# Kernel optimization log

Hardware: AMD Instinct MI355X
Metric: run time of the kernel (lower is better)

## Reference

```python
import jax, jax.numpy as jnp
import numpy as np

B, C, H, W = 4, 128, 128, 128
K = 9          # 3x3 kernel taps
TAU, BETA = 0.5, 10.0


def conv3x3(x, w, b):
    # x: (B,Cin,H,W), w: (Cout,Cin,3,3), stride 1, padding 1
    y = jax.lax.conv_general_dilated(
        x, w, window_strides=(1, 1), padding=((1, 1), (1, 1)),
        dimension_numbers=('NCHW', 'OIHW', 'NCHW'))
    return y + b[None, :, None, None]


def bilinear_sample(x, py, px):
    # x: (B,C,H,W); py,px: (B,K,H,W) fractional coords -> (B,C,K,H,W), zero outside
    Hi, Wi = x.shape[2], x.shape[3]
    y0 = jnp.floor(py); x0 = jnp.floor(px)
    y1 = y0 + 1.0;      x1 = x0 + 1.0
    ly = py - y0; lx = px - x0
    hy = 1.0 - ly; hx = 1.0 - lx
    xf = x.reshape(x.shape[0], x.shape[1], -1)  # (B,C,HW)

    def corner(yc, xc, wgt):
        valid = (yc >= 0) & (yc <= Hi - 1) & (xc >= 0) & (xc <= Wi - 1)
        yi = jnp.clip(yc, 0, Hi - 1).astype(jnp.int32)
        xi = jnp.clip(xc, 0, Wi - 1).astype(jnp.int32)
        idx = (yi * Wi + xi).reshape(yc.shape[0], -1)  # (B, K*H*W)
        g = jax.vmap(lambda f, i: f[:, i])(xf, idx)    # (B,C,K*H*W)
        g = g.reshape(x.shape[0], x.shape[1], *yc.shape[1:])  # (B,C,K,H,W)
        return g * (wgt * valid.astype(wgt.dtype))[:, None]

    return (corner(y0, x0, hy * hx) + corner(y0, x1, hy * lx)
            + corner(y1, x0, ly * hx) + corner(y1, x1, ly * lx))


def modulated_dcn(x, offset, mask, w, b):
    # offset: (B,2K,H,W) layout (dy,dx) per tap; mask: (B,K,H,W)
    Bn, Cn, Hn, Wn = x.shape
    off = offset.reshape(Bn, K, 2, Hn, Wn)
    dy, dx = off[:, :, 0], off[:, :, 1]
    ky, kx = jnp.meshgrid(jnp.arange(3), jnp.arange(3), indexing='ij')
    base_y = (ky.reshape(-1) - 1).astype(x.dtype)  # dilation=1, padding=1, stride=1
    base_x = (kx.reshape(-1) - 1).astype(x.dtype)
    hh = jnp.arange(Hn, dtype=x.dtype)
    ww = jnp.arange(Wn, dtype=x.dtype)
    py = hh[None, None, :, None] + base_y[None, :, None, None] + dy  # (B,K,H,W)
    px = ww[None, None, None, :] + base_x[None, :, None, None] + dx
    samp = bilinear_sample(x, py, px) * mask[:, None]  # (B,C,K,H,W)
    out = jnp.einsum('bckhw,ock->bohw', samp, w.reshape(w.shape[0], w.shape[1], K))
    return out + b[None, :, None, None]


def setup_inputs() -> dict:
    key = jax.random.key(0)
    ks = jax.random.split(key, 8)
    x = jax.random.normal(ks[0], (B, C, H, W), dtype=jnp.float32)
    U = jax.random.uniform(ks[1], (B, 1, H, W), dtype=jnp.float32)
    # conv_offset_mask: (3*K, C+1, 3, 3); small scale -> offsets of O(1) pixel
    w_om = jax.random.normal(ks[2], (3 * K, C + 1, 3, 3), dtype=jnp.float32) * 0.01
    b_om = jnp.zeros((3 * K,), dtype=jnp.float32)
    kaiming = float(np.sqrt(2.0 / (C * 9)))
    w_dcn = jax.random.normal(ks[3], (C, C, 3, 3), dtype=jnp.float32) * kaiming
    b_dcn = jnp.zeros((C,), dtype=jnp.float32)
    w1 = jax.random.normal(ks[4], (C, C, 3, 3), dtype=jnp.float32) * kaiming
    b1 = jnp.zeros((C,), dtype=jnp.float32)
    w2 = jax.random.normal(ks[5], (C, C, 3, 3), dtype=jnp.float32) * float(np.sqrt(1.0 / (C * 9)))
    b2 = jnp.zeros((C,), dtype=jnp.float32)
    return {"x": x, "U": U, "w_om": w_om, "b_om": b_om, "w_dcn": w_dcn,
            "b_dcn": b_dcn, "w1": w1, "b1": b1, "w2": w2, "b2": b2}


def reference(x, U, w_om, b_om, w_dcn, b_dcn, w1, b1, w2, b2):
    U = jnp.clip(U, 0.0, 1.0)
    guide = jnp.concatenate([x, U], axis=1)                # (B,C+1,H,W)
    om = conv3x3(guide, w_om, b_om)                        # (B,3K,H,W)
    offset = om[:, :2 * K]
    mask = 2.0 * jax.nn.sigmoid(om[:, 2 * K:])
    z = modulated_dcn(x, offset, mask, w_dcn, b_dcn)
    r = jax.nn.relu(conv3x3(z, w1, b1))
    r = conv3x3(r, w2, b2)
    gate = jax.nn.sigmoid(BETA * (U - TAU))
    return jax.nn.relu(x + r * gate)
```

## Files before the change

### kernel.cpp

```cpp
#include <hip/hip_runtime.h>
#include <math.h>

typedef unsigned int uint;
typedef unsigned short ushort;
typedef __attribute__((ext_vector_type(8))) __bf16 bf16x8;
typedef __attribute__((ext_vector_type(2))) __bf16 bf16x2;
typedef __attribute__((ext_vector_type(4))) float f32x4;
typedef __attribute__((ext_vector_type(2))) float f32x2;

#define HW 16384

__device__ __forceinline__ ushort f2bf(float f) {
    uint u = __float_as_uint(f);
    u += 0x7fffu + ((u >> 16) & 1u);
    return (ushort)(u >> 16);
}
__device__ __forceinline__ void bhmap(int& b, int& h) {
    int lin = blockIdx.y * (int)gridDim.x + blockIdx.x;
    int n = (lin & 7) * 64 + (lin >> 3);
    h = n & 127;
    b = n >> 7;
}
__device__ __forceinline__ int swz(int row, int chunk) {
    return row * 128 + ((chunk ^ (row & 15)) << 3);
}
__device__ __forceinline__ void gl2lds16(const ushort* g, ushort* l) {
    __builtin_amdgcn_global_load_lds(
        (const __attribute__((address_space(1))) uint*)g,
        (__attribute__((address_space(3))) uint*)l,
        16, 0, 0);
}
__device__ __forceinline__ uint blend2(uint a, uint b, uint c, uint d,
                                       float w00, float w01, float w10, float w11) {
    f32x2 va = { __uint_as_float(a << 16), __uint_as_float(a & 0xffff0000u) };
    f32x2 vb = { __uint_as_float(b << 16), __uint_as_float(b & 0xffff0000u) };
    f32x2 vc = { __uint_as_float(c << 16), __uint_as_float(c & 0xffff0000u) };
    f32x2 vd = { __uint_as_float(d << 16), __uint_as_float(d & 0xffff0000u) };
    f32x2 v = va * w00 + vb * w01 + vc * w10 + vd * w11;
    bf16x2 pk; pk[0] = (__bf16)v[0]; pk[1] = (__bf16)v[1];
    uint r; __builtin_memcpy(&r, &pk, 4);
    return r;
}

__global__ __launch_bounds__(256) void prep_w(
    const float* __restrict__ wd, const float* __restrict__ w1,
    const float* __restrict__ w2, const float* __restrict__ wom,
    ushort* __restrict__ wdt, ushort* __restrict__ w1t,
    ushort* __restrict__ w2t, ushort* __restrict__ womt,
    float* __restrict__ womu)
{
    int i = blockIdx.x * 256 + threadIdx.x;
    if (i < 147456) {
        int k = i >> 14, oc = (i >> 7) & 127, d = i & 127;
        int ci = (((d >> 3) ^ (oc & 15)) << 3) | (d & 7);
        int s = (oc * 128 + ci) * 9 + k;
        wdt[i] = f2bf(wd[s]);
        w1t[i] = f2bf(w1[s]);
        w2t[i] = f2bf(w2[s]);
    }
    if (i < 36864) {
        int k = i >> 12, oc = (i >> 7) & 31, d = i & 127;
        int ci = (((d >> 3) ^ (oc & 15)) << 3) | (d & 7);
        womt[i] = (oc < 27) ? f2bf(wom[(oc * 129 + ci) * 9 + k]) : (ushort)0;
    }
    if (i < 288) {
        int k = i >> 5, oc = i & 31;
        womu[i] = (oc < 27) ? wom[(oc * 129 + 128) * 9 + k] : 0.f;
    }
}

__global__ __launch_bounds__(256) void prep_xt(
    const float* __restrict__ x, ushort* __restrict__ xt)
{
    int b, h; bhmap(b, h);
    const int tid = threadIdx.x;
    __shared__ __align__(16) ushort T[128 * 136];
    const int w0 = tid & 127, cg = tid >> 7;
#pragma unroll 4
    for (int it = 0; it < 64; it++) {
        int c = it * 2 + cg;
        float f = x[((size_t)(b * 128 + c)) * HW + h * 128 + w0];
        T[w0 * 136 + c] = f2bf(f);
    }
    __syncthreads();
    const int w1 = tid >> 1, half = tid & 1;
    uint4* dst = (uint4*)(xt + (((size_t)b * HW) + h * 128 + w1) * 128 + half * 64);
    const uint4* src = (const uint4*)&T[w1 * 136 + half * 64];
#pragma unroll
    for (int c8 = 0; c8 < 8; c8++) dst[c8] = src[c8];
}

__global__ __launch_bounds__(512, 4) void k_om(
    const ushort* __restrict__ xt, const float* __restrict__ U,
    const ushort* __restrict__ womt, const float* __restrict__ womu,
    const float* __restrict__ bom, float* __restrict__ omt)
{
    int b, h; bhmap(b, h);
    const int tid = threadIdx.x;
    const int wid = tid >> 6, lane = tid & 63, lq = lane & 15, quad = lane >> 4;
    const int pixbase = wid * 16;

    __shared__ __align__(16) ushort As[128 * 128];
    __shared__ __align__(16) ushort Bs[32 * 128];
    __shared__ float U3[3 * 130];
    __shared__ float wu[288];

    f32x4 acc[2];
#pragma unroll
    for (int j = 0; j < 2; j++)
#pragma unroll
        for (int r = 0; r < 4; r++) acc[j][r] = 0.f;

    for (int s = tid; s < 390; s += 512) {
        int r = s / 130, c = s % 130, gy = h - 1 + r, gx = c - 1;
        float v = 0.f;
        if ((unsigned)gy < 128u && (unsigned)gx < 128u) {
            v = U[(size_t)b * HW + gy * 128 + gx];
            v = fminf(fmaxf(v, 0.f), 1.f);
        }
        U3[s] = v;
    }
    if (tid < 288) wu[tid] = womu[tid];

    const int arow = tid >> 2, aq = tid & 3;
    for (int t9 = 0; t9 < 9; t9++) {
        int dy = t9 / 3 - 1, dx = t9 % 3 - 1;
        gl2lds16(womt + t9 * 4096 + tid * 8, &Bs[wid * 512]);
        int gy = h + dy, gx = arow + dx;
        if ((unsigned)gy < 128u && (unsigned)gx < 128u) {
            const uint4* src = (const uint4*)(xt + (((size_t)b * HW) + gy * 128 + gx) * 128 + aq * 32);
#pragma unroll
            for (int c = 0; c < 4; c++) *(uint4*)&As[swz(arow, aq * 4 + c)] = src[c];
        } else {
            uint4 zz = {0, 0, 0, 0};
#pragma unroll
            for (int c = 0; c < 4; c++) *(uint4*)&As[swz(arow, aq * 4 + c)] = zz;
        }
        __syncthreads();
#pragma unroll
        for (int kk = 0; kk < 4; kk++) {
            int chunk = kk * 4 + quad;
            bf16x8 av = *(const bf16x8*)&As[swz(pixbase + lq, chunk)];
            bf16x8 bv[2];
#pragma unroll
            for (int j = 0; j < 2; j++) bv[j] = *(const bf16x8*)&Bs[swz(j * 16 + lq, chunk)];
#pragma unroll
            for (int j = 0; j < 2; j++)
                acc[j] = __builtin_amdgcn_mfma_f32_16x16x32_bf16(av, bv[j], acc[j], 0, 0, 0);
        }
        __syncthreads();
    }

#pragma unroll
    for (int j = 0; j < 2; j++) {
        int oc = j * 16 + lq;
        if (oc < 27) {
            float bias = bom[oc];
#pragma unroll
            for (int r = 0; r < 4; r++) {
                int pix = pixbase + quad * 4 + r;
                float v = acc[j][r] + bias;
#pragma unroll
                for (int t = 0; t < 9; t++)
                    v += U3[(t / 3) * 130 + pix + (t % 3)] * wu[t * 32 + oc];
                if (oc >= 18) v = 2.f / (1.f + __expf(-v));
                omt[((size_t)b * HW + h * 128 + pix) * 32 + oc] = v;
            }
        }
    }
}

__global__ __launch_bounds__(512, 4) void k_dcn(
    const ushort* __restrict__ xt, const float* __restrict__ omt,
    const ushort* __restrict__ wdt, const float* __restrict__ bdcn,
    ushort* __restrict__ zt)
{
    int b, h; bhmap(b, h);
    const int tid = threadIdx.x;
    const int wid = tid >> 6, lane = tid & 63, lq = lane & 15, quad = lane >> 4;
    const int pixbase = (wid & 1) * 64, ocbase = (wid >> 1) * 32;

    __shared__ __align__(16) ushort As[128 * 128];
    __shared__ __align__(16) ushort Bs[128 * 128];
    __shared__ __align__(16) int tbl[2][128][8];

    const int sc = lane & 15;
    const int sp = lane >> 4;

    f32x4 acc[4][2];
#pragma unroll
    for (int i = 0; i < 4; i++)
#pragma unroll
        for (int j = 0; j < 2; j++)
#pragma unroll
            for (int r = 0; r < 4; r++) acc[i][j][r] = 0.f;

    const float* omrow = omt + ((size_t)b * HW + h * 128) * 32;
    const ushort* xtb = xt + (size_t)b * HW * 128;

    auto build = [&](int k, int buf) {
        if (tid < 128) {
            int p = tid;
            float dyv = omrow[p * 32 + 2 * k];
            float dxv = omrow[p * 32 + 2 * k + 1];
            float m   = omrow[p * 32 + 18 + k];
            float fy = (float)(h + k / 3 - 1) + dyv;
            float fx = (float)(p + k % 3 - 1) + dxv;
            float y0f = floorf(fy), x0f = floorf(fx);
            float ly = fy - y0f, lx = fx - x0f;
            float hy = 1.f - ly, hx = 1.f - lx;
            bool vy0 = (y0f >= 0.f) && (y0f <= 127.f);
            bool vy1 = (y0f >= -1.f) && (y0f <= 126.f);
            bool vx0 = (x0f >= 0.f) && (x0f <= 127.f);
            bool vx1 = (x0f >= -1.f) && (x0f <= 126.f);
            float w00 = (vy0 && vx0) ? hy * hx * m : 0.f;
            float w01 = (vy0 && vx1) ? hy * lx * m : 0.f;
            float w10 = (vy1 && vx0) ? ly * hx * m : 0.f;
            float w11 = (vy1 && vx1) ? ly * lx * m : 0.f;
            int iy0 = min(max((int)y0f, 0), 127);
            int iy1 = min(max((int)y0f + 1, 0), 127);
            int ix0 = min(max((int)x0f, 0), 127);
            int ix1 = min(max((int)x0f + 1, 0), 127);
            int* tp = &tbl[buf][p][0];
            tp[0] = (iy0 * 128 + ix0) * 128;
            tp[1] = (iy0 * 128 + ix1) * 128;
            tp[2] = (iy1 * 128 + ix0) * 128;
            tp[3] = (iy1 * 128 + ix1) * 128;
            ((float*)tp)[4] = w00; ((float*)tp)[5] = w01;
            ((float*)tp)[6] = w10; ((float*)tp)[7] = w11;
        }
    };

    build(0, 0);
    __syncthreads();

    for (int k = 0; k < 9; k++) {
        const int buf = k & 1;
        {
            const ushort* wsrc = wdt + (size_t)k * 16384;
#pragma unroll
            for (int c = 0; c < 4; c++)
                gl2lds16(wsrc + c * 4096 + tid * 8, &Bs[c * 4096 + wid * 512]);
        }
        const ushort* basep = xtb + sc * 8;
#pragma unroll 2
        for (int r = 0; r < 4; r++) {
            int p = r * 32 + wid * 4 + sp;
            int4 off = *(const int4*)&tbl[buf][p][0];
            f32x4 wv = *(const f32x4*)((const float*)&tbl[buf][p][0] + 4);
            uint4 q00 = *(const uint4*)(basep + off.x);
            uint4 q01 = *(const uint4*)(basep + off.y);
            uint4 q10 = *(const uint4*)(basep + off.z);
            uint4 q11 = *(const uint4*)(basep + off.w);
            uint4 st;
            st.x = blend2(q00.x, q01.x, q10.x, q11.x, wv[0], wv[1], wv[2], wv[3]);
            st.y = blend2(q00.y, q01.y, q10.y, q11.y, wv[0], wv[1], wv[2], wv[3]);
            st.z = blend2(q00.z, q01.z, q10.z, q11.z, wv[0], wv[1], wv[2], wv[3]);
            st.w = blend2(q00.w, q01.w, q10.w, q11.w, wv[0], wv[1], wv[2], wv[3]);
            *(uint4*)&As[swz(p, sc)] = st;
        }
        __syncthreads();
        if (k < 8) build(k + 1, buf ^ 1);
#pragma unroll
        for (int kk = 0; kk < 4; kk++) {
            int chunk = kk * 4 + quad;
            bf16x8 av[4], bv[2];
#pragma unroll
            for (int i = 0; i < 4; i++) av[i] = *(const bf16x8*)&As[swz(pixbase + i * 16 + lq, chunk)];
#pragma unroll
            for (int j = 0; j < 2; j++) bv[j] = *(const bf16x8*)&Bs[swz(ocbase + j * 16 + lq, chunk)];
#pragma unroll
            for (int i = 0; i < 4; i++)
#pragma unroll
                for (int j = 0; j < 2; j++)
                    acc[i][j] = __builtin_amdgcn_mfma_f32_16x16x32_bf16(av[i], bv[j], acc[i][j], 0, 0, 0);
        }
        __syncthreads();
    }

    size_t prow = ((size_t)b * HW + h * 128) * 128;
#pragma unroll
    for (int j = 0; j < 2; j++) {
        int oc = ocbase + j * 16 + lq;
        float bias = bdcn[oc];
#pragma unroll
        for (int i = 0; i < 4; i++)
#pragma unroll
            for (int r = 0; r < 4; r++) {
                int pix = pixbase + i * 16 + quad * 4 + r;
                zt[prow + (size_t)pix * 128 + oc] = f2bf(acc[i][j][r] + bias);
            }
    }
}

__global__ __launch_bounds__(512, 4) void k_conv1(
    const ushort* __restrict__ zt, const ushort* __restrict__ w1t,
    const float* __restrict__ b1, ushort* __restrict__ r1t)
{
    int b, h; bhmap(b, h);
    const int tid = threadIdx.x;
    const int wid = tid >> 6, lane = tid & 63, lq = lane & 15, quad = lane >> 4;
    const int pixbase = (wid & 1) * 64, ocbase = (wid >> 1) * 32;

    __shared__ __align__(16) ushort As[128 * 128];
    __shared__ __align__(16) ushort Bs[128 * 128];

    f32x4 acc[4][2];
#pragma unroll
    for (int i = 0; i < 4; i++)
#pragma unroll
        for (int j = 0; j < 2; j++)
#pragma unroll
            for (int r = 0; r < 4; r++) acc[i][j][r] = 0.f;

    const int row = tid >> 2, q = tid & 3;
    for (int t9 = 0; t9 < 9; t9++) {
        int dy = t9 / 3 - 1, dx = t9 % 3 - 1;
        {
            const ushort* wsrc = w1t + (size_t)t9 * 16384;
#pragma unroll
            for (int c = 0; c < 4; c++)
                gl2lds16(wsrc + c * 4096 + tid * 8, &Bs[c * 4096 + wid * 512]);
        }
        int gy = h + dy, gx = row + dx;
        if ((unsigned)gy < 128u && (unsigned)gx < 128u) {
            const uint4* src = (const uint4*)(zt + (((size_t)b * HW) + gy * 128 + gx) * 128 + q * 32);
#pragma unroll
            for (int c = 0; c < 4; c++) *(uint4*)&As[swz(row, q * 4 + c)] = src[c];
        } else {
            uint4 zz = {0, 0, 0, 0};
#pragma unroll
            for (int c = 0; c < 4; c++) *(uint4*)&As[swz(row, q * 4 + c)] = zz;
        }
        __syncthreads();
#pragma unroll
        for (int kk = 0; kk < 4; kk++) {
            int chunk = kk * 4 + quad;
            bf16x8 av[4], bv[2];
#pragma unroll
            for (int i = 0; i < 4; i++) av[i] = *(const bf16x8*)&As[swz(pixbase + i * 16 + lq, chunk)];
#pragma unroll
            for (int j = 0; j < 2; j++) bv[j] = *(const bf16x8*)&Bs[swz(ocbase + j * 16 + lq, chunk)];
#pragma unroll
            for (int i = 0; i < 4; i++)
#pragma unroll
                for (int j = 0; j < 2; j++)
                    acc[i][j] = __builtin_amdgcn_mfma_f32_16x16x32_bf16(av[i], bv[j], acc[i][j], 0, 0, 0);
        }
        __syncthreads();
    }

    size_t prow = ((size_t)b * HW + h * 128) * 128;
#pragma unroll
    for (int j = 0; j < 2; j++) {
        int oc = ocbase + j * 16 + lq;
        float bias = b1[oc];
#pragma unroll
        for (int i = 0; i < 4; i++)
#pragma unroll
            for (int r = 0; r < 4; r++) {
                int pix = pixbase + i * 16 + quad * 4 + r;
                r1t[prow + (size_t)pix * 128 + oc] = f2bf(fmaxf(acc[i][j][r] + bias, 0.f));
            }
    }
}

__global__ __launch_bounds__(512, 4) void k_conv2(
    const ushort* __restrict__ r1t, const ushort* __restrict__ w2t,
    const float* __restrict__ b2, const float* __restrict__ x,
    const float* __restrict__ U, float* __restrict__ out)
{
    int b, h; bhmap(b, h);
    const int tid = threadIdx.x;
    const int wid = tid >> 6, lane = tid & 63, lq = lane & 15, quad = lane >> 4;
    const int mbase = (wid & 1) * 64;
    const int nbase = (wid >> 1) * 32;

    __shared__ __align__(16) ushort As[128 * 128];
    __shared__ __align__(16) ushort Bs[128 * 128];

    f32x4 acc[4][2];
#pragma unroll
    for (int i = 0; i < 4; i++)
#pragma unroll
        for (int j = 0; j < 2; j++)
#pragma unroll
            for (int r = 0; r < 4; r++) acc[i][j][r] = 0.f;

    const int row = tid >> 2, q = tid & 3;
    for (int t9 = 0; t9 < 9; t9++) {
        int dy = t9 / 3 - 1, dx = t9 % 3 - 1;
        {
            const ushort* wsrc = w2t + (size_t)t9 * 16384;
#pragma unroll
            for (int c = 0; c < 4; c++)
                gl2lds16(wsrc + c * 4096 + tid * 8, &As[c * 4096 + wid * 512]);
        }
        int gy = h + dy, gx = row + dx;
        if ((unsigned)gy < 128u && (unsigned)gx < 128u) {
            const uint4* src = (const uint4*)(r1t + (((size_t)b * HW) + gy * 128 + gx) * 128 + q * 32);
#pragma unroll
            for (int c = 0; c < 4; c++) *(uint4*)&Bs[swz(row, q * 4 + c)] = src[c];
        } else {
            uint4 zz = {0, 0, 0, 0};
#pragma unroll
            for (int c = 0; c < 4; c++) *(uint4*)&Bs[swz(row, q * 4 + c)] = zz;
        }
        __syncthreads();
#pragma unroll
        for (int kk = 0; kk < 4; kk++) {
            int chunk = kk * 4 + quad;
            bf16x8 av[4], bv[2];
#pragma unroll
            for (int i = 0; i < 4; i++) av[i] = *(const bf16x8*)&As[swz(mbase + i * 16 + lq, chunk)];
#pragma unroll
            for (int j = 0; j < 2; j++) bv[j] = *(const bf16x8*)&Bs[swz(nbase + j * 16 + lq, chunk)];
#pragma unroll
            for (int i = 0; i < 4; i++)
#pragma unroll
                for (int j = 0; j < 2; j++)
                    acc[i][j] = __builtin_amdgcn_mfma_f32_16x16x32_bf16(av[i], bv[j], acc[i][j], 0, 0, 0);
        }
        __syncthreads();
    }

#pragma unroll
    for (int j = 0; j < 2; j++) {
        int pix = nbase + j * 16 + lq;
        float u = U[(size_t)b * HW + h * 128 + pix];
        u = fminf(fmaxf(u, 0.f), 1.f);
        float g = 1.f / (1.f + __expf(-10.f * (u - 0.5f)));
#pragma unroll
        for (int i = 0; i < 4; i++) {
            f32x4 b4 = *(const f32x4*)&b2[mbase + i * 16 + quad * 4];
#pragma unroll
            for (int r = 0; r < 4; r++) {
                int oc = mbase + i * 16 + quad * 4 + r;
                size_t idx = ((size_t)(b * 128 + oc)) * HW + h * 128 + pix;
                float v = acc[i][j][r] + b4[r];
                out[idx] = fmaxf(x[idx] + v * g, 0.f);
            }
        }
    }
}

extern "C" void kernel_launch(void* const* d_in, const int* in_sizes, int n_in,
                              void* d_out, int out_size, void* d_ws, size_t ws_size,
                              hipStream_t stream)
{
    const float* x     = (const float*)d_in[0];
    const float* U     = (const float*)d_in[1];
    const float* w_om  = (const float*)d_in[2];
    const float* b_om  = (const float*)d_in[3];
    const float* w_dcn = (const float*)d_in[4];
    const float* b_dcn = (const float*)d_in[5];
    const float* w1    = (const float*)d_in[6];
    const float* b1    = (const float*)d_in[7];
    const float* w2    = (const float*)d_in[8];
    const float* b2    = (const float*)d_in[9];
    float* out = (float*)d_out;

    char* p = (char*)d_ws;
    ushort* xt   = (ushort*)p; p += (size_t)4 * HW * 128 * 2;
    ushort* zt   = (ushort*)p; p += (size_t)4 * HW * 128 * 2;
    ushort* r1t  = (ushort*)p; p += (size_t)4 * HW * 128 * 2;
    float*  omt  = (float*)p;  p += (size_t)4 * HW * 32 * 4;
    ushort* wdt  = (ushort*)p; p += 147456 * 2;
    ushort* w1t  = (ushort*)p; p += 147456 * 2;
    ushort* w2t  = (ushort*)p; p += 147456 * 2;
    ushort* womt = (ushort*)p; p += 36864 * 2;
    float*  womu = (float*)p;  p += 288 * 4;

    prep_w<<<576, 256, 0, stream>>>(w_dcn, w1, w2, w_om, wdt, w1t, w2t, womt, womu);
    prep_xt<<<dim3(128, 4), 256, 0, stream>>>(x, xt);
    k_om<<<dim3(128, 4), 512, 0, stream>>>(xt, U, womt, womu, b_om, omt);
    k_dcn<<<dim3(128, 4), 512, 0, stream>>>(xt, omt, wdt, b_dcn, zt);
    k_conv1<<<dim3(128, 4), 512, 0, stream>>>(zt, w1t, b1, r1t);
    k_conv2<<<dim3(128, 4), 512, 0, stream>>>(r1t, w2t, b2, x, U, out);
}
```

Measured before the change: 220.3 us.

## Reuse haloed input row across dx taps and stream conv1 weights into registers

conv1 now loads one input row per dy with a two-pixel halo (130 rows) into LDS and reuses it for all three dx taps by shifting the row index, instead of reloading the tile for each of the nine taps. Weights are no longer staged in LDS. Each lane reads its B fragments straight from global memory into double-buffered registers, prefetching the next tap's weights while the current tap's MFMAs run. This cuts global-to-LDS traffic and barriers from nine to three per block and halves LDS use. In exchange it raises register pressure and relies on weight reads being served from cache.

```diff
diff --git a/kernel.cpp b/kernel.cpp
--- a/kernel.cpp
+++ b/kernel.cpp
@@ -302,8 +302,7 @@
     const int wid = tid >> 6, lane = tid & 63, lq = lane & 15, quad = lane >> 4;
     const int pixbase = (wid & 1) * 64, ocbase = (wid >> 1) * 32;
 
-    __shared__ __align__(16) ushort As[128 * 128];
-    __shared__ __align__(16) ushort Bs[128 * 128];
+    __shared__ __align__(16) ushort As[130 * 128];
 
     f32x4 acc[4][2];
 #pragma unroll
@@ -313,39 +312,50 @@
 #pragma unroll
             for (int r = 0; r < 4; r++) acc[i][j][r] = 0.f;
 
-    const int row = tid >> 2, q = tid & 3;
-    for (int t9 = 0; t9 < 9; t9++) {
-        int dy = t9 / 3 - 1, dx = t9 % 3 - 1;
-        {
-            const ushort* wsrc = w1t + (size_t)t9 * 16384;
-#pragma unroll
-            for (int c = 0; c < 4; c++)
-                gl2lds16(wsrc + c * 4096 + tid * 8, &Bs[c * 4096 + wid * 512]);
-        }
-        int gy = h + dy, gx = row + dx;
-        if ((unsigned)gy < 128u && (unsigned)gx < 128u) {
-            const uint4* src = (const uint4*)(zt + (((size_t)b * HW) + gy * 128 + gx) * 128 + q * 32);
-#pragma unroll
-            for (int c = 0; c < 4; c++) *(uint4*)&As[swz(row, q * 4 + c)] = src[c];
-        } else {
-            uint4 zz = {0, 0, 0, 0};
-#pragma unroll
-            for (int c = 0; c < 4; c++) *(uint4*)&As[swz(row, q * 4 + c)] = zz;
-        }
-        __syncthreads();
-#pragma unroll
-        for (int kk = 0; kk < 4; kk++) {
-            int chunk = kk * 4 + quad;
-            bf16x8 av[4], bv[2];
-#pragma unroll
-            for (int i = 0; i < 4; i++) av[i] = *(const bf16x8*)&As[swz(pixbase + i * 16 + lq, chunk)];
-#pragma unroll
-            for (int j = 0; j < 2; j++) bv[j] = *(const bf16x8*)&Bs[swz(ocbase + j * 16 + lq, chunk)];
-#pragma unroll
-            for (int i = 0; i < 4; i++)
-#pragma unroll
-                for (int j = 0; j < 2; j++)
-                    acc[i][j] = __builtin_amdgcn_mfma_f32_16x16x32_bf16(av[i], bv[j], acc[i][j], 0, 0, 0);
+    const ushort* wbase = w1t + (ocbase + lq) * 128;
+    auto ldbv = [&](bf16x8 (&dst)[2][4], int t9) {
+#pragma unroll
+        for (int j = 0; j < 2; j++)
+#pragma unroll
+            for (int kk = 0; kk < 4; kk++)
+                dst[j][kk] = *(const bf16x8*)(wbase + t9 * 16384 + j * 2048
+                                              + (((kk * 4 + quad) ^ lq) << 3));
+    };
+
+    bf16x8 bvA[2][4], bvB[2][4];
+    ldbv(bvA, 0);
+
+    const size_t zb = (size_t)b * HW * 128;
+#pragma unroll
+    for (int dyi = 0; dyi < 3; dyi++) {
+        int gy = h + dyi - 1;
+        for (int c = tid; c < 2080; c += 512) {
+            int r = c >> 4, ch = c & 15, gx = r - 1;
+            uint4 v = {0, 0, 0, 0};
+            if ((unsigned)gy < 128u && (unsigned)gx < 128u)
+                v = *(const uint4*)(zt + zb + ((size_t)gy * 128 + gx) * 128 + ch * 8);
+            *(uint4*)&As[swz(r, ch)] = v;
+        }
+        __syncthreads();
+#pragma unroll
+        for (int dx = 0; dx < 3; dx++) {
+            const int t9 = dyi * 3 + dx;
+            bf16x8 (&cur)[2][4] = (t9 & 1) ? bvB : bvA;
+            bf16x8 (&nxt)[2][4] = (t9 & 1) ? bvA : bvB;
+            if (t9 < 8) ldbv(nxt, t9 + 1);
+#pragma unroll
+            for (int kk = 0; kk < 4; kk++) {
+                int chunk = kk * 4 + quad;
+                bf16x8 av[4];
+#pragma unroll
+                for (int i = 0; i < 4; i++)
+                    av[i] = *(const bf16x8*)&As[swz(pixbase + i * 16 + lq + dx, chunk)];
+#pragma unroll
+                for (int i = 0; i < 4; i++)
+#pragma unroll
+                    for (int j = 0; j < 2; j++)
+                        acc[i][j] = __builtin_amdgcn_mfma_f32_16x16x32_bf16(av[i], cur[j][kk], acc[i][j], 0, 0, 0);
+            }
         }
         __syncthreads();
     }
```

Result: slower. 228.4 us (+3.7%).

## Reuse one haloed input row across the three horizontal taps in offset conv

Applied to the files above, without the earlier changes.

The offset/mask conv kernel now loads each input row once with a one-pixel halo (130 pixels) into shared memory and serves all three horizontal taps from it by shifting the row index. Weights for the three taps are staged together. This cuts global loads and barriers from nine per tap to three per kernel row. In exchange it uses more LDS (haloed A tile plus three B tiles), which may reduce occupancy at 4 blocks per CU.

```diff
diff --git a/kernel.cpp b/kernel.cpp
--- a/kernel.cpp
+++ b/kernel.cpp
@@ -100,8 +100,8 @@
     const int wid = tid >> 6, lane = tid & 63, lq = lane & 15, quad = lane >> 4;
     const int pixbase = wid * 16;
 
-    __shared__ __align__(16) ushort As[128 * 128];
-    __shared__ __align__(16) ushort Bs[32 * 128];
+    __shared__ __align__(16) ushort As[130 * 128];
+    __shared__ __align__(16) ushort Bs[3][32 * 128];
     __shared__ float U3[3 * 130];
     __shared__ float wu[288];
 
@@ -122,31 +122,34 @@
     }
     if (tid < 288) wu[tid] = womu[tid];
 
-    const int arow = tid >> 2, aq = tid & 3;
-    for (int t9 = 0; t9 < 9; t9++) {
-        int dy = t9 / 3 - 1, dx = t9 % 3 - 1;
-        gl2lds16(womt + t9 * 4096 + tid * 8, &Bs[wid * 512]);
-        int gy = h + dy, gx = arow + dx;
-        if ((unsigned)gy < 128u && (unsigned)gx < 128u) {
-            const uint4* src = (const uint4*)(xt + (((size_t)b * HW) + gy * 128 + gx) * 128 + aq * 32);
-#pragma unroll
-            for (int c = 0; c < 4; c++) *(uint4*)&As[swz(arow, aq * 4 + c)] = src[c];
-        } else {
-            uint4 zz = {0, 0, 0, 0};
-#pragma unroll
-            for (int c = 0; c < 4; c++) *(uint4*)&As[swz(arow, aq * 4 + c)] = zz;
-        }
-        __syncthreads();
-#pragma unroll
-        for (int kk = 0; kk < 4; kk++) {
-            int chunk = kk * 4 + quad;
-            bf16x8 av = *(const bf16x8*)&As[swz(pixbase + lq, chunk)];
-            bf16x8 bv[2];
-#pragma unroll
-            for (int j = 0; j < 2; j++) bv[j] = *(const bf16x8*)&Bs[swz(j * 16 + lq, chunk)];
-#pragma unroll
-            for (int j = 0; j < 2; j++)
-                acc[j] = __builtin_amdgcn_mfma_f32_16x16x32_bf16(av, bv[j], acc[j], 0, 0, 0);
+    const size_t xb = (size_t)b * HW * 128;
+#pragma unroll
+    for (int dyi = 0; dyi < 3; dyi++) {
+        int gy = h + dyi - 1;
+        for (int c = tid; c < 2080; c += 512) {
+            int r = c >> 4, ch = c & 15, gx = r - 1;
+            uint4 v = {0, 0, 0, 0};
+            if ((unsigned)gy < 128u && (unsigned)gx < 128u)
+                v = *(const uint4*)(xt + xb + ((size_t)gy * 128 + gx) * 128 + ch * 8);
+            *(uint4*)&As[swz(r, ch)] = v;
+        }
+#pragma unroll
+        for (int t = 0; t < 3; t++)
+            gl2lds16(womt + (dyi * 3 + t) * 4096 + tid * 8, &Bs[t][wid * 512]);
+        __syncthreads();
+#pragma unroll
+        for (int dx = 0; dx < 3; dx++) {
+#pragma unroll
+            for (int kk = 0; kk < 4; kk++) {
+                int chunk = kk * 4 + quad;
+                bf16x8 av = *(const bf16x8*)&As[swz(pixbase + lq + dx, chunk)];
+                bf16x8 bv[2];
+#pragma unroll
+                for (int j = 0; j < 2; j++) bv[j] = *(const bf16x8*)&Bs[dx][swz(j * 16 + lq, chunk)];
+#pragma unroll
+                for (int j = 0; j < 2; j++)
+                    acc[j] = __builtin_amdgcn_mfma_f32_16x16x32_bf16(av, bv[j], acc[j], 0, 0, 0);
+            }
         }
         __syncthreads();
     }
```

Result: no change. 216.0 us (-1.9%).
